# Optimization experiments

Measured on AMD Instinct MI355X. Metric: run time of the kernel, lower is better.

Reference implementation:

```python
import jax, jax.numpy as jnp
import numpy as np

B, D_IN, H1, H2, D_OUT = 1024, 2048, 4096, 4096, 1024

def setup_inputs() -> dict:
    key = jax.random.key(0)
    ks = jax.random.split(key, 8)
    scale = lambda fan_in: 1.0 / np.sqrt(fan_in)
    x  = jax.random.normal(ks[0], (B, D_IN), dtype=jnp.float32)
    W1 = jax.random.normal(ks[1], (H1, D_IN), dtype=jnp.float32) * scale(D_IN)
    b1 = jax.random.normal(ks[2], (H1,), dtype=jnp.float32) * scale(D_IN)
    W2 = jax.random.normal(ks[3], (H2, H1), dtype=jnp.float32) * scale(H1)
    b2 = jax.random.normal(ks[4], (H2,), dtype=jnp.float32) * scale(H1)
    W3 = jax.random.normal(ks[5], (D_OUT, H2), dtype=jnp.float32) * scale(H2)
    b3 = jax.random.normal(ks[6], (D_OUT,), dtype=jnp.float32) * scale(H2)
    b_taus = jnp.array([2.0, 1.0, 0.5], dtype=jnp.float32)
    return {"x": x, "W1": W1, "b1": b1, "W2": W2, "b2": b2, "W3": W3, "b3": b3, "b_taus": b_taus, "T": 10}

def reference(x, W1, b1, W2, b2, W3, b3, b_taus, T):
    # x: [B, D_IN] (already flat). betas are scalar sigmoid gates, constant over time.
    beta1, beta2, beta3 = jax.nn.sigmoid(b_taus)
    s1 = jnp.zeros((x.shape[0], W1.shape[0]), dtype=x.dtype)
    s2 = jnp.zeros((x.shape[0], W2.shape[0]), dtype=x.dtype)
    s3 = jnp.zeros((x.shape[0], W3.shape[0]), dtype=x.dtype)

    def step(carry, _):
        s1, s2, s3 = carry
        d1 = jax.nn.relu(x @ W1.T + b1)
        s1 = beta1 * s1 + (1 - beta1) * d1
        d2 = jax.nn.relu(s1 @ W2.T + b2)
        s2 = beta2 * s2 + (1 - beta2) * d2
        d3 = s2 @ W3.T + b3
        s3 = beta3 * s3 + (1 - beta3) * d3
        return (s1, s2, s3), None

    (s1, s2, s3), _ = jax.lax.scan(step, (s1, s2, s3), None, length=T)
    return s3
```

## Files before the change

### kernel.cpp

```cpp
#include <hip/hip_runtime.h>
#include <hip/hip_bf16.h>
#include <stdint.h>

#define AS_GLOBAL __attribute__((address_space(1)))
#define AS_LDS    __attribute__((address_space(3)))

typedef __attribute__((ext_vector_type(8))) short  bf16x8;
typedef __attribute__((ext_vector_type(4))) float  f32x4;
typedef __attribute__((ext_vector_type(4))) short  s16x4;
typedef __attribute__((ext_vector_type(8))) short  s16x8;

__device__ __forceinline__ void gload_lds16(const void* g, void* l) {
    __builtin_amdgcn_global_load_lds((AS_GLOBAL const void*)g, (AS_LDS void*)l, 16, 0, 0);
}

__device__ __forceinline__ void cast_pair(const float* __restrict__ s,
                                          __hip_bfloat16* __restrict__ d, long p) {
    f32x4 a = ((const f32x4*)s)[p * 2];
    f32x4 b = ((const f32x4*)s)[p * 2 + 1];
    union { s16x8 p8; __hip_bfloat16 h[8]; } u;
    u.h[0] = __float2bfloat16(a.x); u.h[1] = __float2bfloat16(a.y);
    u.h[2] = __float2bfloat16(a.z); u.h[3] = __float2bfloat16(a.w);
    u.h[4] = __float2bfloat16(b.x); u.h[5] = __float2bfloat16(b.y);
    u.h[6] = __float2bfloat16(b.z); u.h[7] = __float2bfloat16(b.w);
    ((s16x8*)d)[p] = u.p8;
}

__global__ void cast_a_k(const float* __restrict__ x,  __hip_bfloat16* __restrict__ xb,
                         const float* __restrict__ W1, __hip_bfloat16* __restrict__ W1b) {
    const long nx = 262144, ntot = 1310720, stride = 1280 * 256;
    long t = (long)blockIdx.x * 256 + threadIdx.x;
    for (long p = t; p < ntot; p += stride) {
        if (p < nx) cast_pair(x, xb, p);
        else        cast_pair(W1, W1b, p - nx);
    }
}

template <int FUSECAST>
__global__ __launch_bounds__(256, 4)
void gemm_btk(const __hip_bfloat16* __restrict__ A,
              const __hip_bfloat16* __restrict__ Bm,
              __hip_bfloat16* __restrict__ P,
              const int M, const int N, const int kchunk, const int S,
              const float* __restrict__ cs1, __hip_bfloat16* __restrict__ cd1, const long cn1,
              const float* __restrict__ cs2, __hip_bfloat16* __restrict__ cd2, const long cn2)
{
    __shared__ __hip_bfloat16 As[128 * 64];
    __shared__ __hip_bfloat16 Bs[128 * 64];

    const int tid = threadIdx.x;
    const int bn = blockIdx.x, bm = blockIdx.y, z = blockIdx.z;

    if (FUSECAST && z < FUSECAST) {
        const long nb     = (long)gridDim.x * gridDim.y;
        const long stride = FUSECAST * nb * 256;
        long t = ((long)z * nb + (long)bm * gridDim.x + bn) * 256 + tid;
        const long ntot = cn1 + cn2;
        for (long p = t; p < ntot; p += stride) {
            if (p < cn1) cast_pair(cs1, cd1, p);
            else         cast_pair(cs2, cd2, p - cn1);
        }
        return;
    }
    const int kz = z - FUSECAST;

    const int lane = tid & 63;
    const int wave = tid >> 6;
    const int wm   = wave >> 1, wn = wave & 1;
    const int lm   = lane & 15, lq = lane >> 4;

    const int K  = kchunk * S;
    const int k0 = kz * kchunk;

    const int rlo  = lane >> 3;
    const int gsw8 = (((lane & 7) ^ rlo) << 3);

    const __hip_bfloat16* Ag = A  + (size_t)(bm * 128) * K;
    const __hip_bfloat16* Bg = Bm + (size_t)(bn * 128) * K;

    f32x4 acc[4][4];
    #pragma unroll
    for (int i = 0; i < 4; ++i)
        #pragma unroll
        for (int j = 0; j < 4; ++j)
            acc[i][j] = (f32x4){0.f, 0.f, 0.f, 0.f};

    for (int kt = k0; kt < k0 + kchunk; kt += 64) {
        __syncthreads();
        #pragma unroll
        for (int c = 0; c < 4; ++c) {
            const int chunk = wave * 4 + c;
            const int row   = chunk * 8 + rlo;
            gload_lds16(Ag + (size_t)row * K + kt + gsw8, As + chunk * 512);
            gload_lds16(Bg + (size_t)row * K + kt + gsw8, Bs + chunk * 512);
        }
        __syncthreads();
        #pragma unroll
        for (int kk = 0; kk < 2; ++kk) {
            const int sl = (((kk * 4 + lq) ^ (lm & 7)) << 3);
            bf16x8 af[4], bq[4];
            #pragma unroll
            for (int i = 0; i < 4; ++i)
                af[i] = *(const bf16x8*)(As + (wm * 64 + i * 16 + lm) * 64 + sl);
            #pragma unroll
            for (int j = 0; j < 4; ++j)
                bq[j] = *(const bf16x8*)(Bs + (wn * 64 + j * 16 + lm) * 64 + sl);
            #pragma unroll
            for (int i = 0; i < 4; ++i)
                #pragma unroll
                for (int j = 0; j < 4; ++j)
                    acc[i][j] = __builtin_amdgcn_mfma_f32_16x16x32_bf16(af[i], bq[j], acc[i][j], 0, 0, 0);
        }
    }

    __hip_bfloat16* Pz = P + (size_t)kz * M * N;
    const int row0 = bm * 128 + wm * 64;
    const int colb = bn * 128 + wn * 64 + lm;
    #pragma unroll
    for (int j = 0; j < 4; ++j) {
        const int col = colb + j * 16;
        #pragma unroll
        for (int i = 0; i < 4; ++i)
            #pragma unroll
            for (int r = 0; r < 4; ++r) {
                const int row = row0 + i * 16 + lq * 4 + r;
                Pz[(size_t)row * N + col] = __float2bfloat16(acc[i][j][r]);
            }
    }
}

template <int TT>
__device__ __forceinline__ void tcollapse_coef(float be1, float be2, float be3,
                                               float* __restrict__ c, float* __restrict__ w) {
    float g[TT + 1];
    g[TT] = 1.f;
    float p3 = 1.f;
    #pragma unroll
    for (int u = TT - 1; u >= 1; --u) {
        p3 *= be3;
        g[u] = be2 * g[u + 1] + p3;
    }
    const float s = (1.f - be2) * (1.f - be3);
    float p1 = 1.f;
    #pragma unroll
    for (int u = 1; u <= TT; ++u) {
        p1 *= be1;
        c[u - 1] = 1.f - p1;
        w[u - 1] = s * g[u];
    }
}

template <int MODE>
__global__ void reduce_k(const __hip_bfloat16* __restrict__ P, const int S,
                         void* __restrict__ outv, const long MN, const int N,
                         const float* __restrict__ bias,
                         const float* __restrict__ b_taus,
                         const int* __restrict__ Tp)
{
    long i8 = (long)blockIdx.x * 256 + threadIdx.x;
    long i  = i8 * 8;
    float a[8] = {0.f, 0.f, 0.f, 0.f, 0.f, 0.f, 0.f, 0.f};
    for (int s = 0; s < S; ++s) {
        union { s16x8 p8; __hip_bfloat16 h[8]; } u;
        u.p8 = *(const s16x8*)(P + (size_t)s * MN + i);
        #pragma unroll
        for (int c = 0; c < 8; ++c) a[c] += __bfloat162float(u.h[c]);
    }
    const int col = (int)(i % N);
    float bb[8];
    #pragma unroll
    for (int c = 0; c < 8; ++c) bb[c] = bias[col + c];

    if constexpr (MODE == 0) {
        union { s16x8 p8; __hip_bfloat16 h[8]; } u;
        #pragma unroll
        for (int c = 0; c < 8; ++c)
            u.h[c] = __float2bfloat16(fmaxf(a[c] + bb[c], 0.f));
        ((s16x8*)outv)[i8] = u.p8;
    } else if constexpr (MODE == 1) {
        const int   T   = *Tp;
        const float be1 = 1.f / (1.f + expf(-b_taus[0]));
        const float be2 = 1.f / (1.f + expf(-b_taus[1]));
        const float be3 = 1.f / (1.f + expf(-b_taus[2]));
        union { s16x8 p8; __hip_bfloat16 h[8]; } u;
        if (T == 10) {
            float c10[10], w10[10];
            tcollapse_coef<10>(be1, be2, be3, c10, w10);
            #pragma unroll
            for (int c = 0; c < 8; ++c) {
                float za = 0.f;
                #pragma unroll
                for (int t = 0; t < 10; ++t)
                    za += w10[t] * fmaxf(fmaf(c10[t], a[c], bb[c]), 0.f);
                u.h[c] = __float2bfloat16(za);
            }
        } else {
            #pragma unroll
            for (int c = 0; c < 8; ++c) {
                float p1 = 1.f, s2 = 0.f, za = 0.f;
                for (int t = 0; t < T; ++t) {
                    p1 *= be1;
                    const float d2 = fmaxf(fmaf(1.f - p1, a[c], bb[c]), 0.f);
                    s2 = be2 * s2 + (1.f - be2) * d2;
                    za = be3 * za + (1.f - be3) * s2;
                }
                u.h[c] = __float2bfloat16(za);
            }
        }
        ((s16x8*)outv)[i8] = u.p8;
    } else {
        const int   T   = *Tp;
        const float be3 = 1.f / (1.f + expf(-b_taus[2]));
        float g = 0.f;
        for (int t = 0; t < T; ++t) g = be3 * g + (1.f - be3);
        f32x4 o0, o1;
        o0.x = a[0] + g * bb[0]; o0.y = a[1] + g * bb[1];
        o0.z = a[2] + g * bb[2]; o0.w = a[3] + g * bb[3];
        o1.x = a[4] + g * bb[4]; o1.y = a[5] + g * bb[5];
        o1.z = a[6] + g * bb[6]; o1.w = a[7] + g * bb[7];
        ((f32x4*)outv)[i8 * 2]     = o0;
        ((f32x4*)outv)[i8 * 2 + 1] = o1;
    }
}

extern "C" void kernel_launch(void* const* d_in, const int* in_sizes, int n_in,
                              void* d_out, int out_size, void* d_ws, size_t ws_size,
                              hipStream_t stream) {
    const float* x      = (const float*)d_in[0];
    const float* W1     = (const float*)d_in[1];
    const float* b1     = (const float*)d_in[2];
    const float* W2     = (const float*)d_in[3];
    const float* b2     = (const float*)d_in[4];
    const float* W3     = (const float*)d_in[5];
    const float* b3     = (const float*)d_in[6];
    const float* b_taus = (const float*)d_in[7];
    const int*   Tp     = (const int*)d_in[8];

    const int B = 1024, DIN = 2048, H1 = 4096, H2 = 4096, DOUT = 1024;
    const long MB = 1024 * 1024;

    char* ws = (char*)d_ws;
    __hip_bfloat16* xb  = (__hip_bfloat16*)(ws + 0);
    __hip_bfloat16* W1b = (__hip_bfloat16*)(ws + 4 * MB);
    __hip_bfloat16* W2b = (__hip_bfloat16*)(ws + 20 * MB);
    __hip_bfloat16* W3b = (__hip_bfloat16*)(ws + 52 * MB);
    __hip_bfloat16* D1b = (__hip_bfloat16*)(ws + 60 * MB);
    __hip_bfloat16* Sb  = (__hip_bfloat16*)(ws + 68 * MB);
    __hip_bfloat16* Pb  = (__hip_bfloat16*)(ws + 76 * MB);

    cast_a_k<<<dim3(1280), dim3(256), 0, stream>>>(x, xb, W1, W1b);

    gemm_btk<1><<<dim3(H1 / 128, B / 128, 1 + 4), 256, 0, stream>>>(
        xb, W1b, Pb, B, H1, DIN / 4, 4,
        W2, W2b, (long)H2 * H1 / 8, W3, W3b, (long)DOUT * H2 / 8);
    reduce_k<0><<<dim3(2048), 256, 0, stream>>>(Pb, 4, (void*)D1b, (long)B * H1, H1, b1, nullptr, nullptr);

    gemm_btk<0><<<dim3(H2 / 128, B / 128, 4), 256, 0, stream>>>(
        D1b, W2b, Pb, B, H2, H1 / 4, 4, nullptr, nullptr, 0, nullptr, nullptr, 0);
    reduce_k<1><<<dim3(2048), 256, 0, stream>>>(Pb, 4, (void*)Sb, (long)B * H2, H2, b2, b_taus, Tp);

    gemm_btk<0><<<dim3(DOUT / 128, B / 128, 16), 256, 0, stream>>>(
        Sb, W3b, Pb, B, DOUT, H2 / 16, 16, nullptr, nullptr, 0, nullptr, nullptr, 0);
    reduce_k<2><<<dim3(512), 256, 0, stream>>>(Pb, 16, d_out, (long)B * DOUT, DOUT, b3, b_taus, Tp);
}
```

Before: 265.6 us.

## Move all weight casts into one kernel and retune split-K factors per layer

All four fp32-to-bf16 casts (x, W1, W2, W3) now run in a single standalone kernel instead of casting W2/W3 in extra z-slices of the first GEMM. The first GEMM's split-K drops from 4 to 2 and the third GEMM's from 16 to 8, which shrinks the partial-sum buffers the reduce kernels must read. This gives up overlapping the W2/W3 cast with GEMM1 compute in exchange for simpler GEMMs and less reduction traffic, at the cost of fewer blocks in GEMM1 and GEMM3.

```diff
diff --git a/kernel.cpp b/kernel.cpp
--- a/kernel.cpp
+++ b/kernel.cpp
@@ -7,7 +7,6 @@
 
 typedef __attribute__((ext_vector_type(8))) short  bf16x8;
 typedef __attribute__((ext_vector_type(4))) float  f32x4;
-typedef __attribute__((ext_vector_type(4))) short  s16x4;
 typedef __attribute__((ext_vector_type(8))) short  s16x8;
 
 __device__ __forceinline__ void gload_lds16(const void* g, void* l) {
@@ -26,43 +25,32 @@
     ((s16x8*)d)[p] = u.p8;
 }
 
-__global__ void cast_a_k(const float* __restrict__ x,  __hip_bfloat16* __restrict__ xb,
-                         const float* __restrict__ W1, __hip_bfloat16* __restrict__ W1b) {
-    const long nx = 262144, ntot = 1310720, stride = 1280 * 256;
-    long t = (long)blockIdx.x * 256 + threadIdx.x;
-    for (long p = t; p < ntot; p += stride) {
-        if (p < nx) cast_pair(x, xb, p);
-        else        cast_pair(W1, W1b, p - nx);
-    }
-}
-
-template <int FUSECAST>
+__global__ void cast_all_k(const float* __restrict__ x,  __hip_bfloat16* __restrict__ xb,
+                           const float* __restrict__ W1, __hip_bfloat16* __restrict__ W1b,
+                           const float* __restrict__ W2, __hip_bfloat16* __restrict__ W2b,
+                           const float* __restrict__ W3, __hip_bfloat16* __restrict__ W3b) {
+    const long n0 = 262144, n1 = n0 + 1048576, n2 = n1 + 2097152, n3 = n2 + 524288;
+    const long stride = 2048L * 256;
+    for (long p = (long)blockIdx.x * 256 + threadIdx.x; p < n3; p += stride) {
+        if      (p < n0) cast_pair(x,  xb,  p);
+        else if (p < n1) cast_pair(W1, W1b, p - n0);
+        else if (p < n2) cast_pair(W2, W2b, p - n1);
+        else             cast_pair(W3, W3b, p - n2);
+    }
+}
+
+template <int TAG>
 __global__ __launch_bounds__(256, 4)
-void gemm_btk(const __hip_bfloat16* __restrict__ A,
-              const __hip_bfloat16* __restrict__ Bm,
-              __hip_bfloat16* __restrict__ P,
-              const int M, const int N, const int kchunk, const int S,
-              const float* __restrict__ cs1, __hip_bfloat16* __restrict__ cd1, const long cn1,
-              const float* __restrict__ cs2, __hip_bfloat16* __restrict__ cd2, const long cn2)
+void gemm_l(const __hip_bfloat16* __restrict__ A,
+            const __hip_bfloat16* __restrict__ Bm,
+            __hip_bfloat16* __restrict__ P,
+            const int M, const int N, const int kchunk, const int S)
 {
     __shared__ __hip_bfloat16 As[128 * 64];
     __shared__ __hip_bfloat16 Bs[128 * 64];
 
     const int tid = threadIdx.x;
-    const int bn = blockIdx.x, bm = blockIdx.y, z = blockIdx.z;
-
-    if (FUSECAST && z < FUSECAST) {
-        const long nb     = (long)gridDim.x * gridDim.y;
-        const long stride = FUSECAST * nb * 256;
-        long t = ((long)z * nb + (long)bm * gridDim.x + bn) * 256 + tid;
-        const long ntot = cn1 + cn2;
-        for (long p = t; p < ntot; p += stride) {
-            if (p < cn1) cast_pair(cs1, cd1, p);
-            else         cast_pair(cs2, cd2, p - cn1);
-        }
-        return;
-    }
-    const int kz = z - FUSECAST;
+    const int bn = blockIdx.x, bm = blockIdx.y, kz = blockIdx.z;
 
     const int lane = tid & 63;
     const int wave = tid >> 6;
@@ -248,18 +236,17 @@
     __hip_bfloat16* Sb  = (__hip_bfloat16*)(ws + 68 * MB);
     __hip_bfloat16* Pb  = (__hip_bfloat16*)(ws + 76 * MB);
 
-    cast_a_k<<<dim3(1280), dim3(256), 0, stream>>>(x, xb, W1, W1b);
-
-    gemm_btk<1><<<dim3(H1 / 128, B / 128, 1 + 4), 256, 0, stream>>>(
-        xb, W1b, Pb, B, H1, DIN / 4, 4,
-        W2, W2b, (long)H2 * H1 / 8, W3, W3b, (long)DOUT * H2 / 8);
-    reduce_k<0><<<dim3(2048), 256, 0, stream>>>(Pb, 4, (void*)D1b, (long)B * H1, H1, b1, nullptr, nullptr);
-
-    gemm_btk<0><<<dim3(H2 / 128, B / 128, 4), 256, 0, stream>>>(
-        D1b, W2b, Pb, B, H2, H1 / 4, 4, nullptr, nullptr, 0, nullptr, nullptr, 0);
+    cast_all_k<<<dim3(2048), dim3(256), 0, stream>>>(x, xb, W1, W1b, W2, W2b, W3, W3b);
+
+    gemm_l<1><<<dim3(H1 / 128, B / 128, 2), 256, 0, stream>>>(
+        xb, W1b, Pb, B, H1, DIN / 2, 2);
+    reduce_k<0><<<dim3(2048), 256, 0, stream>>>(Pb, 2, (void*)D1b, (long)B * H1, H1, b1, nullptr, nullptr);
+
+    gemm_l<2><<<dim3(H2 / 128, B / 128, 4), 256, 0, stream>>>(
+        D1b, W2b, Pb, B, H2, H1 / 4, 4);
     reduce_k<1><<<dim3(2048), 256, 0, stream>>>(Pb, 4, (void*)Sb, (long)B * H2, H2, b2, b_taus, Tp);
 
-    gemm_btk<0><<<dim3(DOUT / 128, B / 128, 16), 256, 0, stream>>>(
-        Sb, W3b, Pb, B, DOUT, H2 / 16, 16, nullptr, nullptr, 0, nullptr, nullptr, 0);
-    reduce_k<2><<<dim3(512), 256, 0, stream>>>(Pb, 16, d_out, (long)B * DOUT, DOUT, b3, b_taus, Tp);
-}
+    gemm_l<3><<<dim3(DOUT / 128, B / 128, 8), 256, 0, stream>>>(
+        Sb, W3b, Pb, B, DOUT, H2 / 8, 8);
+    reduce_k<2><<<dim3(512), 256, 0, stream>>>(Pb, 8, d_out, (long)B * DOUT, DOUT, b3, b_taus, Tp);
+}
```

Result: no change. 260.9 us (-1.8%).

## Add 256x256 double-buffered 8-wave GEMM for layer 2 and cut split-K factors

Applied to the files above, without the earlier changes.

Adds a new GEMM kernel with 256x256 tiles, 512 threads, double-buffered LDS staging and phased prefetch interleaved with MFMA under raised wave priority, and uses it for the large H1xH2 layer. The layer-1 and layer-3 split-K factors are halved (4→2, 16→8) and the launch-bounds occupancy hint on the old kernel drops from 4 to 3. The goal is more data reuse per tile, overlap of global loads with compute, and less partial-sum traffic in the reductions. The cost is higher LDS and register use per block and fewer blocks in flight.

```diff
diff --git a/kernel.cpp b/kernel.cpp
--- a/kernel.cpp
+++ b/kernel.cpp
@@ -7,7 +7,6 @@
 
 typedef __attribute__((ext_vector_type(8))) short  bf16x8;
 typedef __attribute__((ext_vector_type(4))) float  f32x4;
-typedef __attribute__((ext_vector_type(4))) short  s16x4;
 typedef __attribute__((ext_vector_type(8))) short  s16x8;
 
 __device__ __forceinline__ void gload_lds16(const void* g, void* l) {
@@ -37,7 +36,7 @@
 }
 
 template <int FUSECAST>
-__global__ __launch_bounds__(256, 4)
+__global__ __launch_bounds__(256, 3)
 void gemm_btk(const __hip_bfloat16* __restrict__ A,
               const __hip_bfloat16* __restrict__ Bm,
               __hip_bfloat16* __restrict__ P,
@@ -121,6 +120,128 @@
         const int col = colb + j * 16;
         #pragma unroll
         for (int i = 0; i < 4; ++i)
+            #pragma unroll
+            for (int r = 0; r < 4; ++r) {
+                const int row = row0 + i * 16 + lq * 4 + r;
+                Pz[(size_t)row * N + col] = __float2bfloat16(acc[i][j][r]);
+            }
+    }
+}
+
+__global__ __launch_bounds__(512, 2)
+void gemm8p(const __hip_bfloat16* __restrict__ A,
+            const __hip_bfloat16* __restrict__ Bm,
+            __hip_bfloat16* __restrict__ P,
+            const int M, const int N, const int kchunk, const int S)
+{
+    __shared__ __hip_bfloat16 As[2][256 * 64];
+    __shared__ __hip_bfloat16 Bs[2][256 * 64];
+
+    const int tid  = threadIdx.x;
+    const int bn   = blockIdx.x, bm = blockIdx.y, kz = blockIdx.z;
+    const int lane = tid & 63;
+    const int wave = tid >> 6;
+    const int wm   = wave >> 2;
+    const int wn   = wave & 3;
+    const int lm   = lane & 15, lq = lane >> 4;
+
+    const int K  = kchunk * S;
+    const int k0 = kz * kchunk;
+    const int nt = kchunk >> 6;
+
+    const int rlo  = lane >> 3;
+    const int gsw8 = (((lane & 7) ^ rlo) << 3);
+
+    const __hip_bfloat16* Ag = A  + (size_t)(bm * 256) * K;
+    const __hip_bfloat16* Bg = Bm + (size_t)(bn * 256) * K;
+
+    f32x4 acc[8][4];
+    #pragma unroll
+    for (int i = 0; i < 8; ++i)
+        #pragma unroll
+        for (int j = 0; j < 4; ++j)
+            acc[i][j] = (f32x4){0.f, 0.f, 0.f, 0.f};
+
+    auto stageA = [&](int d, int kt) {
+        #pragma unroll
+        for (int c = 0; c < 4; ++c) {
+            const int chunk = wave * 4 + c;
+            const int row   = chunk * 8 + rlo;
+            gload_lds16(Ag + (size_t)row * K + kt + gsw8, &As[d][chunk * 512]);
+        }
+    };
+    auto stageB = [&](int d, int kt) {
+        #pragma unroll
+        for (int c = 0; c < 4; ++c) {
+            const int chunk = wave * 4 + c;
+            const int row   = chunk * 8 + rlo;
+            gload_lds16(Bg + (size_t)row * K + kt + gsw8, &Bs[d][chunk * 512]);
+        }
+    };
+
+#define PHASE(KK_, IH_, D_)                                                        \
+    {                                                                              \
+        const int sl = ((((KK_) * 4 + lq) ^ (lm & 7)) << 3);                       \
+        bf16x8 af[4], bq[4];                                                       \
+        _Pragma("unroll")                                                          \
+        for (int i2 = 0; i2 < 4; ++i2)                                             \
+            af[i2] = *(const bf16x8*)(&As[D_][(wm * 128 + ((IH_) * 4 + i2) * 16 + lm) * 64 + sl]); \
+        _Pragma("unroll")                                                          \
+        for (int j = 0; j < 4; ++j)                                                \
+            bq[j] = *(const bf16x8*)(&Bs[D_][(wn * 64 + j * 16 + lm) * 64 + sl]);  \
+        __builtin_amdgcn_s_setprio(1);                                             \
+        _Pragma("unroll")                                                          \
+        for (int i2 = 0; i2 < 4; ++i2)                                             \
+            _Pragma("unroll")                                                      \
+            for (int j = 0; j < 4; ++j)                                            \
+                acc[(IH_) * 4 + i2][j] =                                           \
+                    __builtin_amdgcn_mfma_f32_16x16x32_bf16(af[i2], bq[j],         \
+                                                            acc[(IH_) * 4 + i2][j], 0, 0, 0); \
+        __builtin_amdgcn_s_setprio(0);                                             \
+    }
+
+    stageA(0, k0);
+    stageB(0, k0);
+    __syncthreads();
+
+    int cur = 0;
+    for (int t = 0; t < nt; ++t) {
+        const int ktn  = k0 + (t + 1) * 64;
+        const bool pre = (t + 1 < nt);
+        if (cur == 0) {
+            if (pre) stageA(1, ktn);
+            PHASE(0, 0, 0)
+            __builtin_amdgcn_s_barrier();
+            if (pre) stageB(1, ktn);
+            PHASE(0, 1, 0)
+            __builtin_amdgcn_s_barrier();
+            PHASE(1, 0, 0)
+            __builtin_amdgcn_s_barrier();
+            PHASE(1, 1, 0)
+        } else {
+            if (pre) stageA(0, ktn);
+            PHASE(0, 0, 1)
+            __builtin_amdgcn_s_barrier();
+            if (pre) stageB(0, ktn);
+            PHASE(0, 1, 1)
+            __builtin_amdgcn_s_barrier();
+            PHASE(1, 0, 1)
+            __builtin_amdgcn_s_barrier();
+            PHASE(1, 1, 1)
+        }
+        __syncthreads();
+        cur ^= 1;
+    }
+#undef PHASE
+
+    __hip_bfloat16* Pz = P + (size_t)kz * M * N;
+    const int row0 = bm * 256 + wm * 128;
+    const int colb = bn * 256 + wn * 64 + lm;
+    #pragma unroll
+    for (int j = 0; j < 4; ++j) {
+        const int col = colb + j * 16;
+        #pragma unroll
+        for (int i = 0; i < 8; ++i)
             #pragma unroll
             for (int r = 0; r < 4; ++r) {
                 const int row = row0 + i * 16 + lq * 4 + r;
@@ -250,16 +371,16 @@
 
     cast_a_k<<<dim3(1280), dim3(256), 0, stream>>>(x, xb, W1, W1b);
 
-    gemm_btk<1><<<dim3(H1 / 128, B / 128, 1 + 4), 256, 0, stream>>>(
-        xb, W1b, Pb, B, H1, DIN / 4, 4,
+    gemm_btk<1><<<dim3(H1 / 128, B / 128, 1 + 2), 256, 0, stream>>>(
+        xb, W1b, Pb, B, H1, DIN / 2, 2,
         W2, W2b, (long)H2 * H1 / 8, W3, W3b, (long)DOUT * H2 / 8);
-    reduce_k<0><<<dim3(2048), 256, 0, stream>>>(Pb, 4, (void*)D1b, (long)B * H1, H1, b1, nullptr, nullptr);
-
-    gemm_btk<0><<<dim3(H2 / 128, B / 128, 4), 256, 0, stream>>>(
-        D1b, W2b, Pb, B, H2, H1 / 4, 4, nullptr, nullptr, 0, nullptr, nullptr, 0);
+    reduce_k<0><<<dim3(2048), 256, 0, stream>>>(Pb, 2, (void*)D1b, (long)B * H1, H1, b1, nullptr, nullptr);
+
+    gemm8p<<<dim3(H2 / 256, B / 256, 4), 512, 0, stream>>>(
+        D1b, W2b, Pb, B, H2, H1 / 4, 4);
     reduce_k<1><<<dim3(2048), 256, 0, stream>>>(Pb, 4, (void*)Sb, (long)B * H2, H2, b2, b_taus, Tp);
 
-    gemm_btk<0><<<dim3(DOUT / 128, B / 128, 16), 256, 0, stream>>>(
-        Sb, W3b, Pb, B, DOUT, H2 / 16, 16, nullptr, nullptr, 0, nullptr, nullptr, 0);
-    reduce_k<2><<<dim3(512), 256, 0, stream>>>(Pb, 16, d_out, (long)B * DOUT, DOUT, b3, b_taus, Tp);
-}
+    gemm_btk<0><<<dim3(DOUT / 128, B / 128, 8), 256, 0, stream>>>(
+        Sb, W3b, Pb, B, DOUT, H2 / 8, 8, nullptr, nullptr, 0, nullptr, nullptr, 0);
+    reduce_k<2><<<dim3(512), 256, 0, stream>>>(Pb, 8, d_out, (long)B * DOUT, DOUT, b3, b_taus, Tp);
+}
```

Result: slower. 456.1 us (+71.7%).
